# Optimization experiments

Hardware: AMD Instinct MI355X
Metric: run time of the kernel (lower is better)

Reference implementation:

```python
import jax, jax.numpy as jnp
import numpy as np

N_MOD = 2      # len(l_matrix)
N_SUB = 4096   # each l_matrix entry
DIM = 64
K = 20
ALPHA = 3.0
N = N_MOD * N_SUB  # 8192 total nodes


def setup_inputs() -> dict:
    key = jax.random.key(0)
    k1, k2, k3, k4 = jax.random.split(key, 4)
    nmat = N_MOD * N_MOD
    emb1 = 0.1 * jax.random.normal(k1, (nmat, N_SUB, DIM), dtype=jnp.float32)
    emb2 = 0.1 * jax.random.normal(k2, (nmat, N_SUB, DIM), dtype=jnp.float32)
    # __init__ sets w1/w2 to identity, b to zeros; perturb slightly so they matter
    eye = jnp.eye(DIM, dtype=jnp.float32)
    w1 = eye[None] + 0.01 * jax.random.normal(k3, (nmat, DIM, DIM), dtype=jnp.float32)
    w2 = eye[None] + 0.01 * jax.random.normal(k4, (nmat, DIM, DIM), dtype=jnp.float32)
    b1 = jnp.zeros((nmat, DIM), dtype=jnp.float32)
    b2 = jnp.zeros((nmat, DIM), dtype=jnp.float32)
    idx = jnp.arange(N, dtype=jnp.int64) if jax.config.jax_enable_x64 else jnp.arange(N, dtype=jnp.int32)
    return {"idx": idx, "emb1": emb1, "emb2": emb2, "w1": w1, "w2": w2, "b1": b1, "b2": b2}


def reference(idx, emb1, emb2, w1, w2, b1, b2):
    # per-block linear: nodevec = emb @ w + b   (batched over the nmatrix blocks)
    v1 = jnp.einsum('knd,kde->kne', emb1, w1) + b1[:, None, :]   # [nmat, N_SUB, DIM]
    v2 = jnp.einsum('kmd,kde->kme', emb2, w2) + b2[:, None, :]
    # per-block score: relu(tanh(alpha * v1 @ v2^T))
    a = jnp.einsum('kne,kme->knm', v1, v2)                       # [nmat, N_SUB, N_SUB]
    blocks = jax.nn.relu(jnp.tanh(ALPHA * a))
    # assemble full adjacency: block (i,j) at index i*n_mod + j
    adj = blocks.reshape(N_MOD, N_MOD, N_SUB, N_SUB)
    adj = adj.transpose(0, 2, 1, 3).reshape(N, N)                # [N, N]
    # row-wise topk mask (mask=1 at topk positions), adj * mask
    vals, cols = jax.lax.top_k(adj, K)                           # [N, K]
    rows = jnp.arange(N)[:, None]
    out = jnp.zeros_like(adj).at[rows, cols].set(vals)
    return out


if __name__ == "__main__":
    out = reference(**setup_inputs())
    print(out.shape, float(out.sum()))
```

## Files before the change

kernel.cpp:

```cpp
#include <hip/hip_runtime.h>
#include <hip/hip_bf16.h>

#define NSUB 4096
#define DIM 64
#define NROW 8192
#define KTOP 20
#define LM 24

typedef unsigned long long u64;
typedef __attribute__((ext_vector_type(8))) short bf16x8;
typedef __attribute__((ext_vector_type(4))) float f32x4;

__global__ __launch_bounds__(256) void k_compute_v(
        const float* __restrict__ emb1, const float* __restrict__ w1,
        const float* __restrict__ b1,
        const float* __restrict__ emb2, const float* __restrict__ w2,
        const float* __restrict__ b2,
        double* __restrict__ V1d, double* __restrict__ V2d,
        unsigned short* __restrict__ V1b, unsigned short* __restrict__ V2b) {
    __shared__ alignas(16) float embS[64 * 64];
    __shared__ alignas(16) float wS[64 * 64];
    __shared__ float bS[64];

    int bx    = blockIdx.x;
    int which = bx >> 8;
    int rem   = bx & 255;
    int k     = rem >> 6;
    int tile  = rem & 63;
    int n0    = tile * 64;

    const float* emb = which ? emb2 : emb1;
    const float* w   = which ? w2 : w1;
    const float* b   = which ? b2 : b1;
    double* Vd = which ? V2d : V1d;
    unsigned short* Vb = which ? V2b : V1b;

    int tid = threadIdx.x;
    const float* esrc = emb + ((size_t)k * NSUB + n0) * DIM;
    const float* wsrc = w + (size_t)k * DIM * DIM;
    for (int t = tid; t < 64 * 64; t += 256) { embS[t] = esrc[t]; wS[t] = wsrc[t]; }
    if (tid < 64) bS[tid] = b[k * 64 + tid];
    __syncthreads();

    int e    = tid & 63;
    int mrow = tid >> 6;

    double accs[16];
#pragma unroll
    for (int it = 0; it < 16; ++it) accs[it] = (double)bS[e];

    for (int dg = 0; dg < 16; ++dg) {
        double wv[4];
#pragma unroll
        for (int q = 0; q < 4; ++q) wv[q] = (double)wS[(dg * 4 + q) * 64 + e];
#pragma unroll
        for (int it = 0; it < 16; ++it) {
            float4 em = *(const float4*)&embS[(mrow * 16 + it) * 64 + dg * 4];
            accs[it] += (double)em.x * wv[0] + (double)em.y * wv[1]
                      + (double)em.z * wv[2] + (double)em.w * wv[3];
        }
    }

#pragma unroll
    for (int it = 0; it < 16; ++it) {
        size_t o = ((size_t)k * NSUB + n0 + mrow * 16 + it) * DIM + e;
        Vd[o] = accs[it];
        __hip_bfloat16 hv = __float2bfloat16((float)accs[it]);
        Vb[o] = *reinterpret_cast<unsigned short*>(&hv);
    }
}

__global__ __launch_bounds__(256) void k_select(const unsigned short* __restrict__ V1b,
                                                const unsigned short* __restrict__ V2b,
                                                int* __restrict__ cand) {
    __shared__ float buf[2][4][16][72];

    int tid = threadIdx.x;
    int l = tid & 63;
    int w = tid >> 6;
    int bx = blockIdx.x;
    int r0 = (bx >> 1) * 16;
    int h  = bx & 1;
    int i  = r0 >> 12;
    int n0 = r0 & (NSUB - 1);
    int kb = 2 * i + h;

    const unsigned short* ap =
        V1b + ((size_t)kb * NSUB + n0 + (l & 15)) * DIM + ((l >> 4) * 8);
    bf16x8 a0 = *(const bf16x8*)ap;
    bf16x8 a1 = *(const bf16x8*)(ap + 32);

    const unsigned short* bbase =
        V2b + ((size_t)kb * NSUB + w * 1024 + (l & 15)) * DIM + ((l >> 4) * 8);

    u64 lst[4], th[4];
    float thf[4];
#pragma unroll
    for (int rr = 0; rr < 4; ++rr) {
        lst[rr] = (l < LM) ? (u64)(LM - l) : 0;
        th[rr] = 1;
        thf[rr] = 1e-38f;
    }

    int qrow = (l >> 4) * 4;

    for (int s = 0; s < 16; ++s) {
        int bi = s & 1;
#pragma unroll
        for (int t = 0; t < 4; ++t) {
            const unsigned short* bp = bbase + (size_t)(s * 64 + t * 16) * DIM;
            bf16x8 b0 = *(const bf16x8*)bp;
            bf16x8 b1 = *(const bf16x8*)(bp + 32);
            f32x4 acc = {0.f, 0.f, 0.f, 0.f};
            acc = __builtin_amdgcn_mfma_f32_16x16x32_bf16(a0, b0, acc, 0, 0, 0);
            acc = __builtin_amdgcn_mfma_f32_16x16x32_bf16(a1, b1, acc, 0, 0, 0);
#pragma unroll
            for (int rg = 0; rg < 4; ++rg)
                buf[bi][w][qrow + rg][t * 16 + (l & 15)] = acc[rg];
        }
        __syncthreads();

#pragma unroll
        for (int rr = 0; rr < 4; ++rr) {
            int row = 4 * w + rr;
            float v0 = buf[bi][0][row][l];
            float v1 = buf[bi][1][row][l];
            float v2 = buf[bi][2][row][l];
            float v3 = buf[bi][3][row][l];
            bool p = (v0 >= thf[rr]) || (v1 >= thf[rr]) ||
                     (v2 >= thf[rr]) || (v3 >= thf[rr]);
            if (__ballot(p)) {
                float vu[4] = {v0, v1, v2, v3};
#pragma unroll
                for (int u = 0; u < 4; ++u) {
                    float vv = vu[u];
                    int c = h * 4096 + u * 1024 + s * 64 + l;
                    u64 cd = (vv > 0.f)
                        ? ((((u64)__float_as_uint(vv)) << 13) | (u64)(8191 - c))
                        : 0ull;
                    while (true) {
                        u64 m = __ballot(cd > th[rr]);
                        if (!m) break;
                        int src = __ffsll((unsigned long long)m) - 1;
                        u64 kk = (u64)__shfl((long long)cd, src);
                        u64 e  = lst[rr];
                        u64 up = (u64)__shfl_up((long long)e, 1);
                        int pos = __popcll(__ballot(e > kk));
                        u64 ne = (l < pos) ? e : ((l == pos) ? kk : up);
                        if (l < LM) lst[rr] = ne;
                        th[rr] = (u64)__shfl((long long)lst[rr], LM - 1);
                        if (l == src) cd = 0;
                    }
                }
                thf[rr] = __uint_as_float((unsigned)(th[rr] >> 13));
            }
        }
    }

    if (l < LM) {
#pragma unroll
        for (int rr = 0; rr < 4; ++rr)
            cand[((size_t)(r0 + 4 * w + rr) * 2 + h) * LM + l] =
                8191 - (int)(lst[rr] & 0x1FFFull);
    }
}

__global__ __launch_bounds__(256) void k_refine(const double* __restrict__ V1d,
                                                const double* __restrict__ V2d,
                                                const int* __restrict__ cand,
                                                int* __restrict__ outIdx,
                                                float* __restrict__ outVal) {
    int tid = threadIdx.x;
    int l = tid & 63, w = tid >> 6;
    int row = blockIdx.x * 4 + w;
    int i = row >> 12, n = row & (NSUB - 1);

    int c = 0;
    if (l < 48) {
        int hh = l / LM, j = l % LM;
        c = cand[((size_t)row * 2 + hh) * LM + j];
    }
    int k = 2 * i + (c >> 12);
    int m = c & (NSUB - 1);

    const double* v1p = V1d + ((size_t)k * NSUB + n) * DIM;
    const double* v2p = V2d + ((size_t)k * NSUB + m) * DIM;
    double a = 0.0;
    for (int d = 0; d < DIM; ++d) a += v1p[d] * v2p[d];

    double av = a > 0.0 ? a : 0.0;
    u64 key = (((u64)__double_as_longlong(av)) & ~0x1FFFull) | (u64)(8191 - c);
    if (l >= 48) key = 0;

    int rank = 0;
    for (int jj = 0; jj < 48; ++jj) {
        u64 kj = (u64)__shfl((long long)key, jj);
        rank += (kj > key || (kj == key && jj < l)) ? 1 : 0;
    }
    if (l < 48 && rank < KTOP) {
        float val = (av > 0.0) ? (float)tanh(3.0 * av) : 0.0f;
        outIdx[(size_t)row * KTOP + rank] = c;
        outVal[(size_t)row * KTOP + rank] = val;
    }
}

__global__ __launch_bounds__(256) void k_write(const int* __restrict__ outIdx,
                                               const float* __restrict__ outVal,
                                               float* __restrict__ out) {
    int t = threadIdx.x;
    size_t base = (size_t)blockIdx.x * 4 * NROW;
    float4 z = {0.f, 0.f, 0.f, 0.f};
    float4* o4 = (float4*)(out + base);
#pragma unroll
    for (int it = 0; it < 32; ++it) o4[it * 256 + t] = z;
    __syncthreads();
    if (t < 4 * KTOP) {
        int row = blockIdx.x * 4 + t / KTOP;
        int c = outIdx[(size_t)blockIdx.x * 4 * KTOP + t];
        float v = outVal[(size_t)blockIdx.x * 4 * KTOP + t];
        out[(size_t)row * NROW + c] = v;
    }
}

extern "C" void kernel_launch(void* const* d_in, const int* in_sizes, int n_in,
                              void* d_out, int out_size, void* d_ws, size_t ws_size,
                              hipStream_t stream) {
    const float* emb1 = (const float*)d_in[1];
    const float* emb2 = (const float*)d_in[2];
    const float* w1   = (const float*)d_in[3];
    const float* w2   = (const float*)d_in[4];
    const float* b1   = (const float*)d_in[5];
    const float* b2   = (const float*)d_in[6];
    float* out = (float*)d_out;

    char* p = (char*)d_out;
    double*         V1d = (double*)p;
    double*         V2d = (double*)(p + (size_t)8 * 1024 * 1024);
    unsigned short* V1b = (unsigned short*)(p + (size_t)16 * 1024 * 1024);
    unsigned short* V2b = (unsigned short*)(p + (size_t)18 * 1024 * 1024);
    int*            candp = (int*)(p + (size_t)20 * 1024 * 1024);

    int*   outIdx = (int*)d_ws;
    float* outVal = (float*)((char*)d_ws + (size_t)NROW * KTOP * sizeof(int));

    hipLaunchKernelGGL(k_compute_v, dim3(512), dim3(256), 0, stream,
                       emb1, w1, b1, emb2, w2, b2, V1d, V2d, V1b, V2b);
    hipLaunchKernelGGL(k_select, dim3(1024), dim3(256), 0, stream, V1b, V2b, candp);
    hipLaunchKernelGGL(k_refine, dim3(2048), dim3(256), 0, stream,
                       V1d, V2d, candp, outIdx, outVal);
    hipLaunchKernelGGL(k_write, dim3(2048), dim3(256), 0, stream,
                       outIdx, outVal, out);
}
```

Measured before the change: 524.9 us.

## Replace serial wave top-k insertion with threshold-estimate and filter passes

The per-row wave-level sorted-list insertion in the selection kernel is replaced by three passes. The first keeps the top-2 scores per 256-column group in registers and merges them with shuffles. The second sorts those 64 values per row to get a lower-bound threshold on the 20th largest, minus a margin for bf16 error. The third recomputes the bf16 MFMA scores and appends columns above that threshold to a per-row candidate list with atomics, which the fp64 refine step then ranks. This removes the serialized ballot/shuffle insertion loops and the LDS round-trip with syncthreads, at the cost of a second GEMM pass, atomics, and a fixed 64-entry candidate cap that could drop true top-k columns if it overflows.

```diff
diff --git a/kernel.cpp b/kernel.cpp
--- a/kernel.cpp
+++ b/kernel.cpp
@@ -5,11 +5,14 @@
 #define DIM 64
 #define NROW 8192
 #define KTOP 20
-#define LM 24
+#define CAND 64
 
 typedef unsigned long long u64;
 typedef __attribute__((ext_vector_type(8))) short bf16x8;
 typedef __attribute__((ext_vector_type(4))) float f32x4;
+
+__device__ __forceinline__ unsigned umax(unsigned a, unsigned b) { return a > b ? a : b; }
+__device__ __forceinline__ unsigned umin(unsigned a, unsigned b) { return a < b ? a : b; }
 
 __global__ __launch_bounds__(256) void k_compute_v(
         const float* __restrict__ emb1, const float* __restrict__ w1,
@@ -70,11 +73,9 @@
     }
 }
 
-__global__ __launch_bounds__(256) void k_select(const unsigned short* __restrict__ V1b,
+__global__ __launch_bounds__(256) void k_stage1(const unsigned short* __restrict__ V1b,
                                                 const unsigned short* __restrict__ V2b,
-                                                int* __restrict__ cand) {
-    __shared__ float buf[2][4][16][72];
-
+                                                unsigned int* __restrict__ S1) {
     int tid = threadIdx.x;
     int l = tid & 63;
     int w = tid >> 6;
@@ -93,81 +94,130 @@
     const unsigned short* bbase =
         V2b + ((size_t)kb * NSUB + w * 1024 + (l & 15)) * DIM + ((l >> 4) * 8);
 
-    u64 lst[4], th[4];
-    float thf[4];
-#pragma unroll
-    for (int rr = 0; rr < 4; ++rr) {
-        lst[rr] = (l < LM) ? (u64)(LM - l) : 0;
-        th[rr] = 1;
-        thf[rr] = 1e-38f;
-    }
-
-    int qrow = (l >> 4) * 4;
+    unsigned m1[4] = {0, 0, 0, 0}, m2[4] = {0, 0, 0, 0};
+    int q = l >> 4;
 
     for (int s = 0; s < 16; ++s) {
-        int bi = s & 1;
 #pragma unroll
         for (int t = 0; t < 4; ++t) {
             const unsigned short* bp = bbase + (size_t)(s * 64 + t * 16) * DIM;
             bf16x8 b0 = *(const bf16x8*)bp;
-            bf16x8 b1 = *(const bf16x8*)(bp + 32);
+            bf16x8 b1v = *(const bf16x8*)(bp + 32);
             f32x4 acc = {0.f, 0.f, 0.f, 0.f};
             acc = __builtin_amdgcn_mfma_f32_16x16x32_bf16(a0, b0, acc, 0, 0, 0);
-            acc = __builtin_amdgcn_mfma_f32_16x16x32_bf16(a1, b1, acc, 0, 0, 0);
-#pragma unroll
-            for (int rg = 0; rg < 4; ++rg)
-                buf[bi][w][qrow + rg][t * 16 + (l & 15)] = acc[rg];
-        }
-        __syncthreads();
-
-#pragma unroll
-        for (int rr = 0; rr < 4; ++rr) {
-            int row = 4 * w + rr;
-            float v0 = buf[bi][0][row][l];
-            float v1 = buf[bi][1][row][l];
-            float v2 = buf[bi][2][row][l];
-            float v3 = buf[bi][3][row][l];
-            bool p = (v0 >= thf[rr]) || (v1 >= thf[rr]) ||
-                     (v2 >= thf[rr]) || (v3 >= thf[rr]);
-            if (__ballot(p)) {
-                float vu[4] = {v0, v1, v2, v3};
-#pragma unroll
-                for (int u = 0; u < 4; ++u) {
-                    float vv = vu[u];
-                    int c = h * 4096 + u * 1024 + s * 64 + l;
-                    u64 cd = (vv > 0.f)
-                        ? ((((u64)__float_as_uint(vv)) << 13) | (u64)(8191 - c))
-                        : 0ull;
-                    while (true) {
-                        u64 m = __ballot(cd > th[rr]);
-                        if (!m) break;
-                        int src = __ffsll((unsigned long long)m) - 1;
-                        u64 kk = (u64)__shfl((long long)cd, src);
-                        u64 e  = lst[rr];
-                        u64 up = (u64)__shfl_up((long long)e, 1);
-                        int pos = __popcll(__ballot(e > kk));
-                        u64 ne = (l < pos) ? e : ((l == pos) ? kk : up);
-                        if (l < LM) lst[rr] = ne;
-                        th[rr] = (u64)__shfl((long long)lst[rr], LM - 1);
-                        if (l == src) cd = 0;
-                    }
+            acc = __builtin_amdgcn_mfma_f32_16x16x32_bf16(a1, b1v, acc, 0, 0, 0);
+#pragma unroll
+            for (int r = 0; r < 4; ++r) {
+                unsigned key = __float_as_uint(fmaxf(acc[r], 0.f));
+                m2[r] = umax(m2[r], umin(m1[r], key));
+                m1[r] = umax(m1[r], key);
+            }
+        }
+        if ((s & 3) == 3) {
+#pragma unroll
+            for (int st = 1; st <= 8; st <<= 1) {
+#pragma unroll
+                for (int r = 0; r < 4; ++r) {
+                    unsigned o1 = (unsigned)__shfl_xor((int)m1[r], st);
+                    unsigned o2 = (unsigned)__shfl_xor((int)m2[r], st);
+                    unsigned nm1 = umax(m1[r], o1);
+                    unsigned nm2 = umax(umin(m1[r], o1), umax(m2[r], o2));
+                    m1[r] = nm1; m2[r] = nm2;
                 }
-                thf[rr] = __uint_as_float((unsigned)(th[rr] >> 13));
             }
-        }
-    }
-
-    if (l < LM) {
-#pragma unroll
-        for (int rr = 0; rr < 4; ++rr)
-            cand[((size_t)(r0 + 4 * w + rr) * 2 + h) * LM + l] =
-                8191 - (int)(lst[rr] & 0x1FFFull);
+            if ((l & 15) == 0) {
+                int gblk = h * 16 + w * 4 + (s >> 2);
+#pragma unroll
+                for (int r = 0; r < 4; ++r) {
+                    int rowg = r0 + q * 4 + r;
+                    uint2 v; v.x = m1[r]; v.y = m2[r];
+                    *(uint2*)&S1[(size_t)rowg * 64 + gblk * 2] = v;
+                }
+            }
+#pragma unroll
+            for (int r = 0; r < 4; ++r) { m1[r] = 0; m2[r] = 0; }
+        }
+    }
+}
+
+__global__ __launch_bounds__(256) void k_thresh(const unsigned int* __restrict__ S1,
+                                                float* __restrict__ Lth) {
+    int tid = threadIdx.x;
+    int l = tid & 63, w = tid >> 6;
+    int row = blockIdx.x * 4 + w;
+    unsigned key = S1[(size_t)row * 64 + l];
+#pragma unroll
+    for (int k = 2; k <= 64; k <<= 1) {
+#pragma unroll
+        for (int j = k >> 1; j > 0; j >>= 1) {
+            unsigned other = (unsigned)__shfl_xor((int)key, j);
+            int ixj = l ^ j;
+            bool up = ((l & k) == 0);
+            bool keepMax = ((l > ixj) == up);
+            key = keepMax ? umax(key, other) : umin(key, other);
+        }
+    }
+    if (l == 44) Lth[row] = fmaxf(__uint_as_float(key) - 0.006f, 1e-30f);
+}
+
+__global__ __launch_bounds__(256) void k_filter(const unsigned short* __restrict__ V1b,
+                                                const unsigned short* __restrict__ V2b,
+                                                const float* __restrict__ Lth,
+                                                unsigned int* __restrict__ cnt,
+                                                int* __restrict__ colsG) {
+    __shared__ float Lsh[16];
+    int tid = threadIdx.x;
+    int l = tid & 63;
+    int w = tid >> 6;
+    int bx = blockIdx.x;
+    int r0 = (bx >> 1) * 16;
+    int h  = bx & 1;
+    int i  = r0 >> 12;
+    int n0 = r0 & (NSUB - 1);
+    int kb = 2 * i + h;
+
+    if (tid < 16) Lsh[tid] = Lth[r0 + tid];
+    __syncthreads();
+
+    const unsigned short* ap =
+        V1b + ((size_t)kb * NSUB + n0 + (l & 15)) * DIM + ((l >> 4) * 8);
+    bf16x8 a0 = *(const bf16x8*)ap;
+    bf16x8 a1 = *(const bf16x8*)(ap + 32);
+
+    const unsigned short* bbase =
+        V2b + ((size_t)kb * NSUB + w * 1024 + (l & 15)) * DIM + ((l >> 4) * 8);
+
+    int q = l >> 4;
+    float Lr[4];
+#pragma unroll
+    for (int r = 0; r < 4; ++r) Lr[r] = Lsh[q * 4 + r];
+
+    for (int s = 0; s < 16; ++s) {
+#pragma unroll
+        for (int t = 0; t < 4; ++t) {
+            const unsigned short* bp = bbase + (size_t)(s * 64 + t * 16) * DIM;
+            bf16x8 b0 = *(const bf16x8*)bp;
+            bf16x8 b1v = *(const bf16x8*)(bp + 32);
+            f32x4 acc = {0.f, 0.f, 0.f, 0.f};
+            acc = __builtin_amdgcn_mfma_f32_16x16x32_bf16(a0, b0, acc, 0, 0, 0);
+            acc = __builtin_amdgcn_mfma_f32_16x16x32_bf16(a1, b1v, acc, 0, 0, 0);
+            int c = h * 4096 + w * 1024 + s * 64 + t * 16 + (l & 15);
+#pragma unroll
+            for (int r = 0; r < 4; ++r) {
+                if (acc[r] >= Lr[r]) {
+                    int rowg = r0 + q * 4 + r;
+                    unsigned pos = atomicAdd(&cnt[rowg], 1u);
+                    if (pos < CAND) colsG[(size_t)rowg * CAND + pos] = c;
+                }
+            }
+        }
     }
 }
 
 __global__ __launch_bounds__(256) void k_refine(const double* __restrict__ V1d,
                                                 const double* __restrict__ V2d,
-                                                const int* __restrict__ cand,
+                                                const unsigned int* __restrict__ cnt,
+                                                const int* __restrict__ colsG,
                                                 int* __restrict__ outIdx,
                                                 float* __restrict__ outVal) {
     int tid = threadIdx.x;
@@ -175,11 +225,10 @@
     int row = blockIdx.x * 4 + w;
     int i = row >> 12, n = row & (NSUB - 1);
 
-    int c = 0;
-    if (l < 48) {
-        int hh = l / LM, j = l % LM;
-        c = cand[((size_t)row * 2 + hh) * LM + j];
-    }
+    unsigned cn = cnt[row];
+    if (cn > CAND) cn = CAND;
+    bool valid = (unsigned)l < cn;
+    int c = valid ? colsG[(size_t)row * CAND + l] : 0;
     int k = 2 * i + (c >> 12);
     int m = c & (NSUB - 1);
 
@@ -190,14 +239,14 @@
 
     double av = a > 0.0 ? a : 0.0;
     u64 key = (((u64)__double_as_longlong(av)) & ~0x1FFFull) | (u64)(8191 - c);
-    if (l >= 48) key = 0;
+    if (!valid) key = 0;
 
     int rank = 0;
-    for (int jj = 0; jj < 48; ++jj) {
+    for (int jj = 0; jj < 64; ++jj) {
         u64 kj = (u64)__shfl((long long)key, jj);
         rank += (kj > key || (kj == key && jj < l)) ? 1 : 0;
     }
-    if (l < 48 && rank < KTOP) {
+    if (valid && rank < KTOP) {
         float val = (av > 0.0) ? (float)tanh(3.0 * av) : 0.0f;
         outIdx[(size_t)row * KTOP + rank] = c;
         outVal[(size_t)row * KTOP + rank] = val;
@@ -234,20 +283,26 @@
     float* out = (float*)d_out;
 
     char* p = (char*)d_out;
-    double*         V1d = (double*)p;
-    double*         V2d = (double*)(p + (size_t)8 * 1024 * 1024);
-    unsigned short* V1b = (unsigned short*)(p + (size_t)16 * 1024 * 1024);
-    unsigned short* V2b = (unsigned short*)(p + (size_t)18 * 1024 * 1024);
-    int*            candp = (int*)(p + (size_t)20 * 1024 * 1024);
-
-    int*   outIdx = (int*)d_ws;
-    float* outVal = (float*)((char*)d_ws + (size_t)NROW * KTOP * sizeof(int));
+    double*         V1d   = (double*)p;
+    double*         V2d   = (double*)(p + (size_t)8 * 1024 * 1024);
+    unsigned short* V1b   = (unsigned short*)(p + (size_t)16 * 1024 * 1024);
+    unsigned short* V2b   = (unsigned short*)(p + (size_t)18 * 1024 * 1024);
+    unsigned int*   S1    = (unsigned int*)(p + (size_t)20 * 1024 * 1024);
+    int*            colsG = (int*)(p + (size_t)22 * 1024 * 1024);
+
+    int*          outIdx = (int*)d_ws;
+    float*        outVal = (float*)((char*)d_ws + (size_t)NROW * KTOP * sizeof(int));
+    unsigned int* cntp   = (unsigned int*)((char*)d_ws + (size_t)2 * NROW * KTOP * sizeof(int));
+    float*        Lth    = (float*)((char*)cntp + (size_t)NROW * sizeof(unsigned int));
 
     hipLaunchKernelGGL(k_compute_v, dim3(512), dim3(256), 0, stream,
                        emb1, w1, b1, emb2, w2, b2, V1d, V2d, V1b, V2b);
-    hipLaunchKernelGGL(k_select, dim3(1024), dim3(256), 0, stream, V1b, V2b, candp);
+    hipMemsetAsync(cntp, 0, (size_t)NROW * sizeof(unsigned int), stream);
+    hipLaunchKernelGGL(k_stage1, dim3(1024), dim3(256), 0, stream, V1b, V2b, S1);
+    hipLaunchKernelGGL(k_thresh, dim3(2048), dim3(256), 0, stream, S1, Lth);
+    hipLaunchKernelGGL(k_filter, dim3(1024), dim3(256), 0, stream, V1b, V2b, Lth, cntp, colsG);
     hipLaunchKernelGGL(k_refine, dim3(2048), dim3(256), 0, stream,
-                       V1d, V2d, candp, outIdx, outVal);
+                       V1d, V2d, cntp, colsG, outIdx, outVal);
     hipLaunchKernelGGL(k_write, dim3(2048), dim3(256), 0, stream,
                        outIdx, outVal, out);
 }
```

Measured after the change: 478.3 us. -8.9%, faster.
